# Kernel tuning notes

Hardware: AMD Instinct MI355X
Metric: run time of the kernel (lower is better)

The kernel has to match this reference:

```python
import jax, jax.numpy as jnp
import numpy as np

V, E, H = 32000, 256, 256  # vocab, embed dim, encoder hidden (decoder hidden = 2H)
B, S, T = 64, 32, 32


def gru_cell(x, h, W_ih, W_hh, b_ih, b_hh):
    # PyTorch GRU cell math. x: (B, in), h: (B, Hd)
    gi = x @ W_ih.T + b_ih
    gh = h @ W_hh.T + b_hh
    i_r, i_z, i_n = jnp.split(gi, 3, axis=-1)
    h_r, h_z, h_n = jnp.split(gh, 3, axis=-1)
    r = jax.nn.sigmoid(i_r + h_r)
    z = jax.nn.sigmoid(i_z + h_z)
    n = jnp.tanh(i_n + r * h_n)
    return (1.0 - z) * n + z * h


def setup_inputs() -> dict:
    key = jax.random.key(0)
    ks = jax.random.split(key, 20)
    s = 0.05
    emb_enc = jax.random.normal(ks[0], (V, E), jnp.float32) * s
    emb_enc = emb_enc.at[0].set(0.0)  # padding_idx=0
    emb_dec = jax.random.normal(ks[1], (V, E), jnp.float32) * s
    emb_dec = emb_dec.at[0].set(0.0)
    inp = {
        "src": jax.random.randint(ks[2], (B, S), 0, V),
        "trg": jax.random.randint(ks[3], (B, T), 0, V),
        "emb_enc": emb_enc,
        # encoder bidirectional GRU (single layer)
        "W_ih_f": jax.random.normal(ks[4], (3 * H, E), jnp.float32) * s,
        "W_hh_f": jax.random.normal(ks[5], (3 * H, H), jnp.float32) * s,
        "b_ih_f": jnp.zeros((3 * H,), jnp.float32),
        "b_hh_f": jnp.zeros((3 * H,), jnp.float32),
        "W_ih_b": jax.random.normal(ks[6], (3 * H, E), jnp.float32) * s,
        "W_hh_b": jax.random.normal(ks[7], (3 * H, H), jnp.float32) * s,
        "b_ih_b": jnp.zeros((3 * H,), jnp.float32),
        "b_hh_b": jnp.zeros((3 * H,), jnp.float32),
        "emb_dec": emb_dec,
        # decoder GRU: input E + 2H, hidden 2H
        "W_ih_d": jax.random.normal(ks[8], (3 * 2 * H, E + 2 * H), jnp.float32) * s,
        "W_hh_d": jax.random.normal(ks[9], (3 * 2 * H, 2 * H), jnp.float32) * s,
        "b_ih_d": jnp.zeros((3 * 2 * H,), jnp.float32),
        "b_hh_d": jnp.zeros((3 * 2 * H,), jnp.float32),
        "fc_W": jax.random.normal(ks[10], (V, 2 * H), jnp.float32) * s,
        "fc_b": jnp.zeros((V,), jnp.float32),
    }
    return inp


def _forward(src, trg, emb_enc, W_ih_f, W_hh_f, b_ih_f, b_hh_f,
             W_ih_b, W_hh_b, b_ih_b, b_hh_b, emb_dec,
             W_ih_d, W_hh_d, b_ih_d, b_hh_d, fc_W, fc_b):
    b, s = src.shape
    t = trg.shape[1]
    x = emb_enc[src]                      # (B,S,E)
    xs = jnp.swapaxes(x, 0, 1)            # (S,B,E)
    h0 = jnp.zeros((b, H), x.dtype)

    def fstep(h, xt):
        h = gru_cell(xt, h, W_ih_f, W_hh_f, b_ih_f, b_hh_f)
        return h, None

    def bstep(h, xt):
        h = gru_cell(xt, h, W_ih_b, W_hh_b, b_ih_b, b_hh_b)
        return h, None

    hf, _ = jax.lax.scan(fstep, h0, xs)
    hb, _ = jax.lax.scan(bstep, h0, xs[::-1])
    context = jnp.concatenate([hf, hb], axis=-1)   # (B,2H) = final bidir hidden

    # teacher_forcing_ratio = 1.0 -> decoder input at step t is trg[:, t-1]
    dec_in = jnp.swapaxes(trg[:, :-1], 0, 1)       # (T-1, B)

    def dstep(h, tok):
        xt = jnp.concatenate([emb_dec[tok], context], axis=-1)  # (B, E+2H)
        h = gru_cell(xt, h, W_ih_d, W_hh_d, b_ih_d, b_hh_d)
        logits = h @ fc_W.T + fc_b                              # (B, V)
        return h, logits

    _, logits = jax.lax.scan(dstep, context, dec_in)  # (T-1, B, V)
    logits = jnp.swapaxes(logits, 0, 1)                # (B, T-1, V)
    outputs = jnp.concatenate(
        [jnp.zeros((b, 1, fc_W.shape[0]), logits.dtype), logits], axis=1)
    return outputs


def reference(src, trg, emb_enc, W_ih_f, W_hh_f, b_ih_f, b_hh_f,
              W_ih_b, W_hh_b, b_ih_b, b_hh_b, emb_dec,
              W_ih_d, W_hh_d, b_ih_d, b_hh_d, fc_W, fc_b):
    return _forward(src, trg, emb_enc, W_ih_f, W_hh_f, b_ih_f, b_hh_f,
                    W_ih_b, W_hh_b, b_ih_b, b_hh_b, emb_dec,
                    W_ih_d, W_hh_d, b_ih_d, b_hh_d, fc_W, fc_b)
```

## Files before the change

kernel.cpp:

```cpp
#include <hip/hip_runtime.h>
#include <cmath>

typedef _Float16 f16;
typedef _Float16 f16x4 __attribute__((ext_vector_type(4)));
typedef _Float16 f16x8 __attribute__((ext_vector_type(8)));
typedef float f32x4 __attribute__((ext_vector_type(4)));
typedef unsigned u32x4 __attribute__((ext_vector_type(4)));
typedef unsigned long long u64;


union V4 { u32x4 u; f16x8 h; };

static constexpr size_t OFF_WIHF = 0;
static constexpr size_t OFF_WHHF = OFF_WIHF + 768UL*256*2;
static constexpr size_t OFF_WIHB = OFF_WHHF + 768UL*256*2;
static constexpr size_t OFF_WHHB = OFF_WIHB + 768UL*256*2;
static constexpr size_t OFF_WIHD = OFF_WHHB + 768UL*256*2;
static constexpr size_t OFF_WHHD = OFF_WIHD + 1536UL*768*2;
static constexpr size_t OFF_FCW  = OFF_WHHD + 1536UL*512*2;
static constexpr size_t OFF_XENC = OFF_FCW  + 32000UL*512*2;
static constexpr size_t OFF_XDEC = OFF_XENC + 2048UL*256*2;
static constexpr size_t OFF_GIF  = OFF_XDEC + 1984UL*256*2;
static constexpr size_t OFF_GIB  = OFF_GIF  + 2048UL*768*4;
static constexpr size_t OFF_GITOK= OFF_GIB  + 2048UL*768*4;
static constexpr size_t OFF_CTX32= OFF_GITOK+ 1984UL*1536*4;
static constexpr size_t OFF_CTX16= OFF_CTX32+ 64UL*512*4;
static constexpr size_t OFF_HPP  = OFF_CTX16+ 64UL*512*2;
static constexpr size_t OFF_HALL = OFF_HPP  + 2UL*32*64*256*2;
static constexpr size_t OFF_FLG  = OFF_HALL + 2048UL*512*2;

__device__ __forceinline__ float sigmoidf_(float x) {
  return __builtin_amdgcn_rcpf(1.f + __expf(-x));
}
__device__ __forceinline__ float tanhf_(float x) {
  float xc = fminf(fmaxf(x, -10.f), 10.f);
  float e = __expf(2.f * xc);
  return (e - 1.f) * __builtin_amdgcn_rcpf(e + 1.f);
}

__device__ __forceinline__ void wait_vm0() {
  asm volatile("s_waitcnt vmcnt(0)" ::: "memory");
  __builtin_amdgcn_sched_barrier(0);
}
__device__ __forceinline__ void sth4(f16* p, float a, float b, float c, float d) {
  union { u64 u; f16 h[4]; } t;
  t.h[0] = (f16)a; t.h[1] = (f16)b; t.h[2] = (f16)c; t.h[3] = (f16)d;
  __hip_atomic_store((u64*)p, t.u, __ATOMIC_RELAXED, __HIP_MEMORY_SCOPE_AGENT);
}
__device__ __forceinline__ int ldflag(const int* p) {
  return __hip_atomic_load(p, __ATOMIC_RELAXED, __HIP_MEMORY_SCOPE_AGENT);
}
__device__ __forceinline__ void stflag(int* p, int v) {
  __hip_atomic_store(p, v, __ATOMIC_RELAXED, __HIP_MEMORY_SCOPE_AGENT);
}
__device__ __forceinline__ void pollflags(const int* base, int np, int tgt) {
  int lane = threadIdx.x & 63;
  const int* fp = base + lane * 16;
  for (;;) {
    int v = (lane < np) ? ldflag(fp) : 0x7fffffff;
    if (__all(v >= tgt)) break;
    __builtin_amdgcn_s_sleep(1);
  }
  __builtin_amdgcn_sched_barrier(0);
}

__global__ void k_init(const int* __restrict__ srct, const int* __restrict__ trgt,
                       const float* __restrict__ embe, const float* __restrict__ embd,
                       const float* __restrict__ wihf, const float* __restrict__ whhf,
                       const float* __restrict__ wihb, const float* __restrict__ whhb,
                       const float* __restrict__ wihd, const float* __restrict__ whhd,
                       const float* __restrict__ fcw,
                       f16* dWihf, f16* dWhhf, f16* dWihb, f16* dWhhb,
                       f16* dWihd, f16* dWhhd, f16* dFcw,
                       f16* __restrict__ Xenc, f16* __restrict__ Xdec,
                       f16* __restrict__ hpp, int* __restrict__ flg,
                       float* __restrict__ out) {
  int b = blockIdx.x, tid = threadIdx.x;
  if (b < 1024) {
    long t = (long)b * 256 + tid;
    const long stride = 1024L * 256;
    for (long i = t; i < 4032L * 64; i += stride) {
      int row = (int)(i >> 6), j4 = (int)(i & 63);
      const float* e; f16* d; int tok;
      if (row < 2048) {
        int s = row >> 6, bb = row & 63;
        tok = srct[bb * 32 + s]; e = embe; d = Xenc + (long)row * 256;
      } else {
        int rd = row - 2048; int tt = rd >> 6, bb = rd & 63;
        tok = trgt[bb * 32 + tt]; e = embd; d = Xdec + (long)rd * 256;
      }
      float4 v = ((const float4*)(e + (long)tok * 256))[j4];
      f16x4 o; o.x = (f16)v.x; o.y = (f16)v.y; o.z = (f16)v.z; o.w = (f16)v.w;
      ((f16x4*)d)[j4] = o;
    }
    for (long i = t; i < 64L * 8000; i += stride) {
      long bb = i / 8000, j = i % 8000;
      ((float4*)(out + bb * 1024000L))[j] = make_float4(0.f, 0.f, 0.f, 0.f);
    }
    if (t < 8192) flg[t] = 0;
    u64* P8 = (u64*)hpp;
    if (t < 4096) { P8[t] = 0ULL; P8[131072 + t] = 0ULL; }
  } else {
    long cb = b - 1024;
    const long stride = 4672L * 256;
    for (long i = cb * 256 + tid; i < 4784128L; i += stride) {
      const float* s; f16* d; long j = i;
      if (j < 49152L)        { s = wihf; d = dWihf; }
      else if (j < 98304L)   { s = whhf; d = dWhhf; j -= 49152L; }
      else if (j < 147456L)  { s = wihb; d = dWihb; j -= 98304L; }
      else if (j < 196608L)  { s = whhb; d = dWhhb; j -= 147456L; }
      else if (j < 491520L)  { s = wihd; d = dWihd; j -= 196608L; }
      else if (j < 688128L)  { s = whhd; d = dWhhd; j -= 491520L; }
      else                   { s = fcw;  d = dFcw;  j -= 688128L; }
      float4 v = ((const float4*)s)[j];
      f16x4 o; o.x = (f16)v.x; o.y = (f16)v.y; o.z = (f16)v.z; o.w = (f16)v.w;
      ((f16x4*)d)[j] = o;
    }
  }
}

__device__ __forceinline__ void gemm_body(int bx, int by,
                                          const f16* __restrict__ A, int lda,
                                          const f16* __restrict__ B, int ldb,
                                          const float* __restrict__ bias,
                                          float* __restrict__ C, int ldc, int Ksteps) {
  int m0 = bx * 64, n0 = by * 64;
  int lane = threadIdx.x & 63, w = threadIdx.x >> 6;
  int ar = m0 + w * 16 + (lane & 15);
  int koff = (lane >> 4) * 8;
  f32x4 acc[4] = {};
  for (int ks = 0; ks < Ksteps; ks++) {
    f16x8 a = *(const f16x8*)(A + (size_t)ar * lda + ks * 32 + koff);
#pragma unroll
    for (int ni = 0; ni < 4; ni++) {
      const f16* bp = B + (size_t)(n0 + ni * 16 + (lane & 15)) * ldb + ks * 32 + koff;
      f16x8 bfr = *(const f16x8*)bp;
      acc[ni] = __builtin_amdgcn_mfma_f32_16x16x32_f16(a, bfr, acc[ni], 0, 0, 0);
    }
  }
  int dm = m0 + w * 16 + ((lane >> 4) << 2);
  int dn0 = n0 + (lane & 15);
#pragma unroll
  for (int ni = 0; ni < 4; ni++) {
    int n = dn0 + ni * 16;
    float bv = bias ? bias[n] : 0.f;
#pragma unroll
    for (int r = 0; r < 4; r++) C[(size_t)(dm + r) * ldc + n] = acc[ni][r] + bv;
  }
}

__global__ __launch_bounds__(256) void k_gi(const f16* __restrict__ Xenc, const f16* __restrict__ Xdec,
                                            const f16* __restrict__ Wf, const f16* __restrict__ Wb,
                                            const f16* __restrict__ Wd,
                                            const float* __restrict__ bf, const float* __restrict__ bb,
                                            float* __restrict__ giF, float* __restrict__ giB,
                                            float* __restrict__ giTok) {
  int b = blockIdx.x;
  if (b < 384)      gemm_body(b & 31, b >> 5, Xenc, 256, Wf, 256, bf, giF, 768, 8);
  else if (b < 768) { b -= 384; gemm_body(b & 31, b >> 5, Xenc, 256, Wb, 256, bb, giB, 768, 8); }
  else              { b -= 768; gemm_body(b % 31, b / 31, Xdec, 256, Wd, 768, nullptr, giTok, 1536, 8); }
}

__global__ __launch_bounds__(256, 1) void k_enc(
    const float* __restrict__ giF, const float* __restrict__ giB,
    const f16* __restrict__ WhhF, const f16* __restrict__ WhhB,
    const float* __restrict__ bhhF, const float* __restrict__ bhhB,
    f16* __restrict__ hpp, float* __restrict__ ctx32, f16* __restrict__ ctx16,
    int* __restrict__ flg) {
  __shared__ f16 W[96 * 256];
  int wg = blockIdx.x;
  int dir = wg >> 3, ns = wg & 7;
  int tid = threadIdx.x, lane = tid & 63, wv = tid >> 6;
  int mTile = wv;
  const float* gi = dir ? giB : giF;
  const f16* Whh = dir ? WhhB : WhhF;
  const float* bhh = dir ? bhhB : bhhF;
  f16* hb = hpp + (size_t)dir * (32 * 64 * 256);
  int lo = lane & 15, hi = lane >> 4;
  int m = mTile * 16 + lo;
  int jb0 = ns * 32 + hi * 4;

#pragma unroll
  for (int c = 0; c < 12; c++) {
    int seg = c * 256 + tid;
    int row = seg >> 5, ck = seg & 31;
    int q = row >> 5, ii = row & 31;
    f16x8 v = *(const f16x8*)(Whh + (size_t)(q * 256 + ns * 32 + ii) * 256 + ck * 8);
    int col = (ck * 8) ^ ((row & 7) << 3);
    *(f16x8*)&W[row * 256 + col] = v;
  }
  __syncthreads();

  float4 bh[3][2];
#pragma unroll
  for (int q = 0; q < 3; q++)
#pragma unroll
    for (int i = 0; i < 2; i++)
      bh[q][i] = *(const float4*)(bhh + q * 256 + jb0 + i * 16);

  float4 ho[2] = {};
  float4 gcur[3][2];
  {
    int s0 = dir ? 31 : 0;
    const float* g0 = gi + (size_t)s0 * (64 * 768);
#pragma unroll
    for (int q = 0; q < 3; q++)
#pragma unroll
      for (int i = 0; i < 2; i++)
        gcur[q][i] = *(const float4*)(g0 + (size_t)m * 768 + q * 256 + jb0 + i * 16);
  }
  int* gflags = flg + 4096 + (dir * 4 + mTile) * 128;

  for (int s = 0; s < 32; s++) {
    if (s > 0) pollflags(gflags, 8, s);
    V4 hv[8];
    const char* hb8 = (const char*)hb + ((size_t)s * 16384 + (size_t)m * 256 + hi * 8) * 2;
#pragma unroll
    for (int ks = 0; ks < 8; ks++)
      asm volatile("global_load_dwordx4 %0, %1, off offset:%2 sc0 sc1"
                   : "=&v"(hv[ks].u) : "v"(hb8), "i"(ks * 64));
    wait_vm0();
    f32x4 acc[3][2] = {};
#pragma unroll
    for (int ks = 0; ks < 8; ks++) {
#pragma unroll
      for (int q = 0; q < 3; q++)
#pragma unroll
        for (int i = 0; i < 2; i++) {
          int row = q * 32 + i * 16 + lo;
          int col = (ks * 32 + hi * 8) ^ ((row & 7) << 3);
          f16x8 w = *(const f16x8*)&W[row * 256 + col];
          acc[q][i] = __builtin_amdgcn_mfma_f32_16x16x32_f16(w, hv[ks].h, acc[q][i], 0, 0, 0);
        }
    }
#pragma unroll
    for (int i = 0; i < 2; i++) {
      float hvv[4];
#pragma unroll
      for (int r2 = 0; r2 < 4; r2++) {
        float rg = sigmoidf_(((const float*)&gcur[0][i])[r2] + acc[0][i][r2] + ((const float*)&bh[0][i])[r2]);
        float zg = sigmoidf_(((const float*)&gcur[1][i])[r2] + acc[1][i][r2] + ((const float*)&bh[1][i])[r2]);
        float ng = tanhf_(((const float*)&gcur[2][i])[r2] + rg * (acc[2][i][r2] + ((const float*)&bh[2][i])[r2]));
        float hprev = ((const float*)&ho[i])[r2];
        hvv[r2] = (1.f - zg) * ng + zg * hprev;
        ((float*)&ho[i])[r2] = hvv[r2];
      }
      if (s < 31) sth4(hb + (size_t)(s + 1) * 16384 + m * 256 + jb0 + i * 16,
                       hvv[0], hvv[1], hvv[2], hvv[3]);
    }
    if (s < 31) {
      wait_vm0();
      if (lane == 0) stflag(gflags + ns * 16, s + 1);
      int sn = s + 1;
      int sgin = dir ? (31 - sn) : sn;
      const float* gs = gi + (size_t)sgin * (64 * 768);
#pragma unroll
      for (int q = 0; q < 3; q++)
#pragma unroll
        for (int i = 0; i < 2; i++)
          gcur[q][i] = *(const float4*)(gs + (size_t)m * 768 + q * 256 + jb0 + i * 16);
    }
  }
#pragma unroll
  for (int i = 0; i < 2; i++) {
    int c = dir * 256 + jb0 + i * 16;
    *(float4*)(ctx32 + m * 512 + c) = ho[i];
    union { u64 u; f16 h[4]; } t;
#pragma unroll
    for (int r2 = 0; r2 < 4; r2++) t.h[r2] = (f16)((const float*)&ho[i])[r2];
    *(u64*)(ctx16 + m * 512 + c) = t.u;
  }
}

__global__ __launch_bounds__(256, 1) void k_dec(
    const float* __restrict__ giTok, const f16* __restrict__ Wihd, const float* __restrict__ bihd,
    const f16* __restrict__ Whh, const float* __restrict__ bhh,
    const float* __restrict__ ctx32, const f16* __restrict__ ctx16,
    f16* __restrict__ Hall, int* __restrict__ flg) {
  __shared__ f16 W[48 * 512];
  int cg = blockIdx.x;
  int tid = threadIdx.x, lane = tid & 63, wv = tid >> 6;
  int mTile = wv;
  int lo = lane & 15, hi = lane >> 4;
  int koff = hi * 8;
  int m = mTile * 16 + lo;
  int j0 = cg * 16 + hi * 4;

#pragma unroll
  for (int c = 0; c < 12; c++) {
    int seg = c * 256 + tid;
    int row = seg >> 6, ck = seg & 63;
    int q = row >> 4, ii = row & 15;
    f16x8 v = *(const f16x8*)(Whh + (size_t)(q * 512 + cg * 16 + ii) * 512 + ck * 8);
    int col = (ck * 8) ^ ((row & 7) << 3);
    *(f16x8*)&W[row * 512 + col] = v;
  }

  f32x4 acx[3] = {};
#pragma unroll
  for (int ks = 0; ks < 16; ks++) {
    f16x8 a = *(const f16x8*)(ctx16 + (size_t)m * 512 + ks * 32 + koff);
#pragma unroll
    for (int q = 0; q < 3; q++) {
      f16x8 w = *(const f16x8*)(Wihd + (size_t)(q * 512 + cg * 16 + lo) * 768 + 256 + ks * 32 + koff);
      acx[q] = __builtin_amdgcn_mfma_f32_16x16x32_f16(w, a, acx[q], 0, 0, 0);
    }
  }
  float b0[4], b1[4], bo2[4], bhn[4];
#pragma unroll
  for (int r2 = 0; r2 < 4; r2++) {
    b0[r2]  = acx[0][r2] + bihd[j0 + r2]        + bhh[j0 + r2];
    b1[r2]  = acx[1][r2] + bihd[512 + j0 + r2]  + bhh[512 + j0 + r2];
    bo2[r2] = acx[2][r2] + bihd[1024 + j0 + r2];
    bhn[r2] = bhh[1024 + j0 + r2];
  }
  float4 ho = *(const float4*)(ctx32 + m * 512 + j0);
  float4 gcur[3];
#pragma unroll
  for (int q = 0; q < 3; q++)
    gcur[q] = *(const float4*)(giTok + (size_t)m * 1536 + q * 512 + j0);
  __syncthreads();

  int* gflags = flg + mTile * 512;

  for (int t = 0; t < 31; t++) {
    V4 hv[16];
    if (t == 0) {
      const char* cb = (const char*)ctx16 + ((size_t)m * 512 + hi * 8) * 2;
#pragma unroll
      for (int ks = 0; ks < 16; ks++)
        hv[ks].u = *(const u32x4*)(cb + ks * 64);
    } else {
      pollflags(gflags, 32, t);
      const char* hb8 = (const char*)Hall + ((size_t)(t - 1) * 32768 + (size_t)m * 512 + hi * 8) * 2;
#pragma unroll
      for (int ks = 0; ks < 16; ks++)
        asm volatile("global_load_dwordx4 %0, %1, off offset:%2 sc0 sc1"
                     : "=&v"(hv[ks].u) : "v"(hb8), "i"(ks * 64));
      wait_vm0();
    }
    f32x4 acc[3] = {};
#pragma unroll
    for (int ks = 0; ks < 16; ks++) {
#pragma unroll
      for (int q = 0; q < 3; q++) {
        int row = q * 16 + lo;
        int col = (ks * 32 + hi * 8) ^ ((row & 7) << 3);
        f16x8 w = *(const f16x8*)&W[row * 512 + col];
        acc[q] = __builtin_amdgcn_mfma_f32_16x16x32_f16(w, hv[ks].h, acc[q], 0, 0, 0);
      }
    }
    float hvv[4];
#pragma unroll
    for (int r2 = 0; r2 < 4; r2++) {
      float rg = sigmoidf_(((const float*)&gcur[0])[r2] + acc[0][r2] + b0[r2]);
      float zg = sigmoidf_(((const float*)&gcur[1])[r2] + acc[1][r2] + b1[r2]);
      float ng = tanhf_(((const float*)&gcur[2])[r2] + bo2[r2] + rg * (acc[2][r2] + bhn[r2]));
      float hprev = ((const float*)&ho)[r2];
      hvv[r2] = (1.f - zg) * ng + zg * hprev;
      ((float*)&ho)[r2] = hvv[r2];
    }
    sth4(Hall + (size_t)t * 32768 + (size_t)m * 512 + j0, hvv[0], hvv[1], hvv[2], hvv[3]);
    wait_vm0();
    if (lane == 0) stflag(gflags + cg * 16, t + 1);
    {
      int tn = (t + 1 < 31) ? t + 1 : 30;
      const float* gs = giTok + (size_t)tn * (64 * 1536);
#pragma unroll
      for (int q = 0; q < 3; q++)
        gcur[q] = *(const float4*)(gs + (size_t)m * 1536 + q * 512 + j0);
    }
  }
}

__global__ __launch_bounds__(256, 2) void k_fc(const f16* __restrict__ Hall, const f16* __restrict__ Wfc,
                                               const float* __restrict__ fcb, float* __restrict__ out) {
  __shared__ f16 As[128 * 64];
  __shared__ f16 Bs[128 * 64];
  int bid = blockIdx.x;
  int bx = bid >> 4;
  int by = bid & 15;
  int m0 = by * 128, n0 = bx * 128;
  int tid = threadIdx.x, lane = tid & 63, wv = tid >> 6;
  int wm = wv >> 1, wn = wv & 1;
  f32x4 acc[4][4] = {};
  for (int kk = 0; kk < 8; kk++) {
    f16x8 ra[4], rb[4];
#pragma unroll
    for (int c = 0; c < 4; c++) {
      int seg = c * 256 + tid;
      int row = seg >> 3, ko = (seg & 7) * 8;
      ra[c] = *(const f16x8*)(Hall + (size_t)(m0 + row) * 512 + kk * 64 + ko);
      rb[c] = *(const f16x8*)(Wfc + (size_t)(n0 + row) * 512 + kk * 64 + ko);
    }
    __syncthreads();
#pragma unroll
    for (int c = 0; c < 4; c++) {
      int seg = c * 256 + tid;
      int row = seg >> 3;
      int col = ((seg & 7) * 8) ^ ((row & 7) << 3);
      *(f16x8*)&As[row * 64 + col] = ra[c];
      *(f16x8*)&Bs[row * 64 + col] = rb[c];
    }
    __syncthreads();
#pragma unroll
    for (int ks = 0; ks < 2; ks++) {
      f16x8 af[4], bf[4];
#pragma unroll
      for (int mi = 0; mi < 4; mi++) {
        int row = wm * 64 + mi * 16 + (lane & 15);
        int col = (ks * 32 + (lane >> 4) * 8) ^ ((row & 7) << 3);
        af[mi] = *(const f16x8*)&As[row * 64 + col];
      }
#pragma unroll
      for (int ni = 0; ni < 4; ni++) {
        int row = wn * 64 + ni * 16 + (lane & 15);
        int col = (ks * 32 + (lane >> 4) * 8) ^ ((row & 7) << 3);
        bf[ni] = *(const f16x8*)&Bs[row * 64 + col];
      }
#pragma unroll
      for (int mi = 0; mi < 4; mi++) {
#pragma unroll
        for (int ni = 0; ni < 4; ni++)
          acc[mi][ni] = __builtin_amdgcn_mfma_f32_16x16x32_f16(af[mi], bf[ni], acc[mi][ni], 0, 0, 0);
      }
    }
  }
  int dn0 = n0 + wn * 64 + (lane & 15);
  float bv[4];
#pragma unroll
  for (int ni = 0; ni < 4; ni++) bv[ni] = fcb[dn0 + ni * 16];
#pragma unroll
  for (int mi = 0; mi < 4; mi++) {
    int mbase = m0 + wm * 64 + mi * 16 + ((lane >> 4) << 2);
#pragma unroll
    for (int rr = 0; rr < 4; rr++) {
      int mm = mbase + rr;
      if (mm < 1984) {
        int t = mm >> 6, bb = mm & 63;
        float* orow = out + (size_t)bb * 1024000 + (size_t)(t + 1) * 32000;
#pragma unroll
        for (int ni = 0; ni < 4; ni++) orow[dn0 + ni * 16] = acc[mi][ni][rr] + bv[ni];
      }
    }
  }
}

extern "C" void kernel_launch(void* const* d_in, const int* in_sizes, int n_in,
                              void* d_out, int out_size, void* d_ws, size_t ws_size,
                              hipStream_t stream) {
  const int*   srct = (const int*)d_in[0];
  const int*   trgt = (const int*)d_in[1];
  const float* embe = (const float*)d_in[2];
  const float* wihf = (const float*)d_in[3];
  const float* whhf = (const float*)d_in[4];
  const float* bihf = (const float*)d_in[5];
  const float* bhhf = (const float*)d_in[6];
  const float* wihb = (const float*)d_in[7];
  const float* whhb = (const float*)d_in[8];
  const float* bihb = (const float*)d_in[9];
  const float* bhhb = (const float*)d_in[10];
  const float* embd = (const float*)d_in[11];
  const float* wihd = (const float*)d_in[12];
  const float* whhd = (const float*)d_in[13];
  const float* bihd = (const float*)d_in[14];
  const float* bhhd = (const float*)d_in[15];
  const float* fcw  = (const float*)d_in[16];
  const float* fcb  = (const float*)d_in[17];
  float* out = (float*)d_out;
  char* ws = (char*)d_ws;

  f16* W_ihf = (f16*)(ws + OFF_WIHF);
  f16* W_hhf = (f16*)(ws + OFF_WHHF);
  f16* W_ihb = (f16*)(ws + OFF_WIHB);
  f16* W_hhb = (f16*)(ws + OFF_WHHB);
  f16* W_ihd = (f16*)(ws + OFF_WIHD);
  f16* W_hhd = (f16*)(ws + OFF_WHHD);
  f16* Wfc   = (f16*)(ws + OFF_FCW);
  f16* Xenc  = (f16*)(ws + OFF_XENC);
  f16* Xdec  = (f16*)(ws + OFF_XDEC);
  float* giF   = (float*)(ws + OFF_GIF);
  float* giB   = (float*)(ws + OFF_GIB);
  float* giTok = (float*)(ws + OFF_GITOK);
  float* ctx32 = (float*)(ws + OFF_CTX32);
  f16*   ctx16 = (f16*)(ws + OFF_CTX16);
  f16*   hpp   = (f16*)(ws + OFF_HPP);
  f16*   Hall  = (f16*)(ws + OFF_HALL);
  int*   flg   = (int*)(ws + OFF_FLG);

  k_init<<<5696, 256, 0, stream>>>(srct, trgt, embe, embd,
                                   wihf, whhf, wihb, whhb, wihd, whhd, fcw,
                                   W_ihf, W_hhf, W_ihb, W_hhb, W_ihd, W_hhd, Wfc,
                                   Xenc, Xdec, hpp, flg, out);
  k_gi<<<1512, 256, 0, stream>>>(Xenc, Xdec, W_ihf, W_ihb, W_ihd, bihf, bihb,
                                 giF, giB, giTok);
  k_enc<<<16, 256, 0, stream>>>(giF, giB, W_hhf, W_hhb, bhhf, bhhb, hpp, ctx32, ctx16, flg);
  k_dec<<<32, 256, 0, stream>>>(giTok, W_ihd, bihd, W_hhd, bhhd, ctx32, ctx16, Hall, flg);
  k_fc<<<4000, 256, 0, stream>>>(Hall, Wfc, fcb, out);
}
```

Baseline: 437.9 us.

## Replace flag polling with sentinel-filled hidden buffers for inter-block sync

Removes the per-step flag stores and flag polling in the encoder and decoder recurrences. The hidden-state buffers are pre-filled with an all-ones sentinel, and consumers spin on the data loads themselves until no sentinel remains. This drops one full wait and flag round-trip per timestep from the serial critical path. It relies on 64-bit stores being atomic and on real fp16 values never forming the sentinel pattern. It also adds sentinel initialization traffic in k_init and switches the logits output stores to nontemporal.

```diff
diff --git a/kernel.cpp b/kernel.cpp
--- a/kernel.cpp
+++ b/kernel.cpp
@@ -8,6 +8,7 @@
 typedef unsigned u32x4 __attribute__((ext_vector_type(4)));
 typedef unsigned long long u64;
 
+static constexpr u64 SENT = 0xFFFFFFFFFFFFFFFFULL;
 
 union V4 { u32x4 u; f16x8 h; };
 
@@ -27,7 +28,6 @@
 static constexpr size_t OFF_CTX16= OFF_CTX32+ 64UL*512*4;
 static constexpr size_t OFF_HPP  = OFF_CTX16+ 64UL*512*2;
 static constexpr size_t OFF_HALL = OFF_HPP  + 2UL*32*64*256*2;
-static constexpr size_t OFF_FLG  = OFF_HALL + 2048UL*512*2;
 
 __device__ __forceinline__ float sigmoidf_(float x) {
   return __builtin_amdgcn_rcpf(1.f + __expf(-x));
@@ -46,22 +46,6 @@
   union { u64 u; f16 h[4]; } t;
   t.h[0] = (f16)a; t.h[1] = (f16)b; t.h[2] = (f16)c; t.h[3] = (f16)d;
   __hip_atomic_store((u64*)p, t.u, __ATOMIC_RELAXED, __HIP_MEMORY_SCOPE_AGENT);
-}
-__device__ __forceinline__ int ldflag(const int* p) {
-  return __hip_atomic_load(p, __ATOMIC_RELAXED, __HIP_MEMORY_SCOPE_AGENT);
-}
-__device__ __forceinline__ void stflag(int* p, int v) {
-  __hip_atomic_store(p, v, __ATOMIC_RELAXED, __HIP_MEMORY_SCOPE_AGENT);
-}
-__device__ __forceinline__ void pollflags(const int* base, int np, int tgt) {
-  int lane = threadIdx.x & 63;
-  const int* fp = base + lane * 16;
-  for (;;) {
-    int v = (lane < np) ? ldflag(fp) : 0x7fffffff;
-    if (__all(v >= tgt)) break;
-    __builtin_amdgcn_s_sleep(1);
-  }
-  __builtin_amdgcn_sched_barrier(0);
 }
 
 __global__ void k_init(const int* __restrict__ srct, const int* __restrict__ trgt,
@@ -73,7 +57,7 @@
                        f16* dWihf, f16* dWhhf, f16* dWihb, f16* dWhhb,
                        f16* dWihd, f16* dWhhd, f16* dFcw,
                        f16* __restrict__ Xenc, f16* __restrict__ Xdec,
-                       f16* __restrict__ hpp, int* __restrict__ flg,
+                       f16* __restrict__ hpp, f16* __restrict__ Hall,
                        float* __restrict__ out) {
   int b = blockIdx.x, tid = threadIdx.x;
   if (b < 1024) {
@@ -97,9 +81,11 @@
       long bb = i / 8000, j = i % 8000;
       ((float4*)(out + bb * 1024000L))[j] = make_float4(0.f, 0.f, 0.f, 0.f);
     }
-    if (t < 8192) flg[t] = 0;
+    u64* H8 = (u64*)Hall;
+    if (t < 253952) H8[t] = SENT;
     u64* P8 = (u64*)hpp;
     if (t < 4096) { P8[t] = 0ULL; P8[131072 + t] = 0ULL; }
+    if (t < 126976) { P8[4096 + t] = SENT; P8[131072 + 4096 + t] = SENT; }
   } else {
     long cb = b - 1024;
     const long stride = 4672L * 256;
@@ -165,8 +151,7 @@
     const float* __restrict__ giF, const float* __restrict__ giB,
     const f16* __restrict__ WhhF, const f16* __restrict__ WhhB,
     const float* __restrict__ bhhF, const float* __restrict__ bhhB,
-    f16* __restrict__ hpp, float* __restrict__ ctx32, f16* __restrict__ ctx16,
-    int* __restrict__ flg) {
+    f16* __restrict__ hpp, float* __restrict__ ctx32, f16* __restrict__ ctx16) {
   __shared__ f16 W[96 * 256];
   int wg = blockIdx.x;
   int dir = wg >> 3, ns = wg & 7;
@@ -209,17 +194,25 @@
       for (int i = 0; i < 2; i++)
         gcur[q][i] = *(const float4*)(g0 + (size_t)m * 768 + q * 256 + jb0 + i * 16);
   }
-  int* gflags = flg + 4096 + (dir * 4 + mTile) * 128;
 
   for (int s = 0; s < 32; s++) {
-    if (s > 0) pollflags(gflags, 8, s);
     V4 hv[8];
     const char* hb8 = (const char*)hb + ((size_t)s * 16384 + (size_t)m * 256 + hi * 8) * 2;
-#pragma unroll
-    for (int ks = 0; ks < 8; ks++)
-      asm volatile("global_load_dwordx4 %0, %1, off offset:%2 sc0 sc1"
-                   : "=&v"(hv[ks].u) : "v"(hb8), "i"(ks * 64));
-    wait_vm0();
+    for (;;) {
+#pragma unroll
+      for (int ks = 0; ks < 8; ks++)
+        asm volatile("global_load_dwordx4 %0, %1, off offset:%2 sc0 sc1"
+                     : "=&v"(hv[ks].u) : "v"(hb8), "i"(ks * 64));
+      wait_vm0();
+      unsigned bad = 0;
+#pragma unroll
+      for (int ks = 0; ks < 8; ks++) {
+        bad |= ((hv[ks].u.x & hv[ks].u.y) == 0xFFFFFFFFu);
+        bad |= ((hv[ks].u.z & hv[ks].u.w) == 0xFFFFFFFFu);
+      }
+      if (!__any((int)bad)) break;
+      __builtin_amdgcn_s_sleep(1);
+    }
     f32x4 acc[3][2] = {};
 #pragma unroll
     for (int ks = 0; ks < 8; ks++) {
@@ -249,8 +242,6 @@
                        hvv[0], hvv[1], hvv[2], hvv[3]);
     }
     if (s < 31) {
-      wait_vm0();
-      if (lane == 0) stflag(gflags + ns * 16, s + 1);
       int sn = s + 1;
       int sgin = dir ? (31 - sn) : sn;
       const float* gs = gi + (size_t)sgin * (64 * 768);
@@ -276,7 +267,7 @@
     const float* __restrict__ giTok, const f16* __restrict__ Wihd, const float* __restrict__ bihd,
     const f16* __restrict__ Whh, const float* __restrict__ bhh,
     const float* __restrict__ ctx32, const f16* __restrict__ ctx16,
-    f16* __restrict__ Hall, int* __restrict__ flg) {
+    f16* __restrict__ Hall) {
   __shared__ f16 W[48 * 512];
   int cg = blockIdx.x;
   int tid = threadIdx.x, lane = tid & 63, wv = tid >> 6;
@@ -321,8 +312,6 @@
     gcur[q] = *(const float4*)(giTok + (size_t)m * 1536 + q * 512 + j0);
   __syncthreads();
 
-  int* gflags = flg + mTile * 512;
-
   for (int t = 0; t < 31; t++) {
     V4 hv[16];
     if (t == 0) {
@@ -331,13 +320,22 @@
       for (int ks = 0; ks < 16; ks++)
         hv[ks].u = *(const u32x4*)(cb + ks * 64);
     } else {
-      pollflags(gflags, 32, t);
       const char* hb8 = (const char*)Hall + ((size_t)(t - 1) * 32768 + (size_t)m * 512 + hi * 8) * 2;
-#pragma unroll
-      for (int ks = 0; ks < 16; ks++)
-        asm volatile("global_load_dwordx4 %0, %1, off offset:%2 sc0 sc1"
-                     : "=&v"(hv[ks].u) : "v"(hb8), "i"(ks * 64));
-      wait_vm0();
+      for (;;) {
+#pragma unroll
+        for (int ks = 0; ks < 16; ks++)
+          asm volatile("global_load_dwordx4 %0, %1, off offset:%2 sc0 sc1"
+                       : "=&v"(hv[ks].u) : "v"(hb8), "i"(ks * 64));
+        wait_vm0();
+        unsigned bad = 0;
+#pragma unroll
+        for (int ks = 0; ks < 16; ks++) {
+          bad |= ((hv[ks].u.x & hv[ks].u.y) == 0xFFFFFFFFu);
+          bad |= ((hv[ks].u.z & hv[ks].u.w) == 0xFFFFFFFFu);
+        }
+        if (!__any((int)bad)) break;
+        __builtin_amdgcn_s_sleep(1);
+      }
     }
     f32x4 acc[3] = {};
 #pragma unroll
@@ -361,8 +359,6 @@
       ((float*)&ho)[r2] = hvv[r2];
     }
     sth4(Hall + (size_t)t * 32768 + (size_t)m * 512 + j0, hvv[0], hvv[1], hvv[2], hvv[3]);
-    wait_vm0();
-    if (lane == 0) stflag(gflags + cg * 16, t + 1);
     {
       int tn = (t + 1 < 31) ? t + 1 : 30;
       const float* gs = giTok + (size_t)tn * (64 * 1536);
@@ -440,7 +436,8 @@
         int t = mm >> 6, bb = mm & 63;
         float* orow = out + (size_t)bb * 1024000 + (size_t)(t + 1) * 32000;
 #pragma unroll
-        for (int ni = 0; ni < 4; ni++) orow[dn0 + ni * 16] = acc[mi][ni][rr] + bv[ni];
+        for (int ni = 0; ni < 4; ni++)
+          __builtin_nontemporal_store(acc[mi][ni][rr] + bv[ni], orow + dn0 + ni * 16);
       }
     }
   }
@@ -486,15 +483,14 @@
   f16*   ctx16 = (f16*)(ws + OFF_CTX16);
   f16*   hpp   = (f16*)(ws + OFF_HPP);
   f16*   Hall  = (f16*)(ws + OFF_HALL);
-  int*   flg   = (int*)(ws + OFF_FLG);
 
   k_init<<<5696, 256, 0, stream>>>(srct, trgt, embe, embd,
                                    wihf, whhf, wihb, whhb, wihd, whhd, fcw,
                                    W_ihf, W_hhf, W_ihb, W_hhb, W_ihd, W_hhd, Wfc,
-                                   Xenc, Xdec, hpp, flg, out);
+                                   Xenc, Xdec, hpp, Hall, out);
   k_gi<<<1512, 256, 0, stream>>>(Xenc, Xdec, W_ihf, W_ihb, W_ihd, bihf, bihb,
                                  giF, giB, giTok);
-  k_enc<<<16, 256, 0, stream>>>(giF, giB, W_hhf, W_hhb, bhhf, bhhb, hpp, ctx32, ctx16, flg);
-  k_dec<<<32, 256, 0, stream>>>(giTok, W_ihd, bihd, W_hhd, bhhd, ctx32, ctx16, Hall, flg);
+  k_enc<<<16, 256, 0, stream>>>(giF, giB, W_hhf, W_hhb, bhhf, bhhb, hpp, ctx32, ctx16);
+  k_dec<<<32, 256, 0, stream>>>(giTok, W_ihd, bihd, W_hhd, bhhd, ctx32, ctx16, Hall);
   k_fc<<<4000, 256, 0, stream>>>(Hall, Wfc, fcb, out);
 }
```

Result: faster. 425.8 us (-2.7%).
